# Kernel tuning notes

Measured on AMD Instinct MI355X. Metric: run time of the kernel, lower is better.

Reference implementation:

```python
import jax, jax.numpy as jnp
import numpy as np

N = 100000      # nodes
E = 1600000     # edges (avg degree 16)
IN = 512        # input feature dim
H, C = 8, 8     # conv1: 8 heads x 8 channels (hardcoded in module)
HID = H * C     # 64
OUT = 64        # output classes (conv2: 1 head, no concat)
NEG_SLOPE = 0.2 # PyG GATConv default leaky-relu slope


def setup_inputs() -> dict:
    key = jax.random.key(0)
    ks = jax.random.split(key, 10)
    x = jax.random.normal(ks[0], (N, IN), dtype=jnp.float32)
    edge_index = jax.random.randint(ks[1], (2, E), 0, N, dtype=jnp.int32)
    W1 = jax.random.normal(ks[2], (IN, HID), dtype=jnp.float32) / np.sqrt(IN).astype(np.float32)
    a_src1 = jax.random.normal(ks[3], (H, C), dtype=jnp.float32) * 0.1
    a_dst1 = jax.random.normal(ks[4], (H, C), dtype=jnp.float32) * 0.1
    b1 = jnp.zeros((HID,), dtype=jnp.float32)
    W2 = jax.random.normal(ks[5], (HID, OUT), dtype=jnp.float32) / np.sqrt(HID).astype(np.float32)
    a_src2 = jax.random.normal(ks[6], (1, OUT), dtype=jnp.float32) * 0.1
    a_dst2 = jax.random.normal(ks[7], (1, OUT), dtype=jnp.float32) * 0.1
    b2 = jnp.zeros((OUT,), dtype=jnp.float32)
    return {"x": x, "edge_index": edge_index, "W1": W1, "a_src1": a_src1,
            "a_dst1": a_dst1, "b1": b1, "W2": W2, "a_src2": a_src2,
            "a_dst2": a_dst2, "b2": b2}


def _gat_attend(h, src, dst, a_s, a_d, n_nodes):
    """h: [N,H,C]; src/dst: [E]; a_s/a_d: [H,C] -> aggregated [N,H,C]."""
    # per-node half-scores (PyG decomposition of a^T [Wx_i || Wx_j])
    sc_s = jnp.sum(h * a_s, axis=-1)                       # [N,H]
    sc_d = jnp.sum(h * a_d, axis=-1)                       # [N,H]
    logits = jax.nn.leaky_relu(sc_s[src] + sc_d[dst], NEG_SLOPE)  # [E,H]
    # segment softmax over edges grouped by destination node
    mx = jax.ops.segment_max(logits, dst, num_segments=n_nodes)   # [N,H]
    ex = jnp.exp(logits - mx[dst])                          # [E,H]
    denom = jax.ops.segment_sum(ex, dst, num_segments=n_nodes)    # [N,H]
    alpha = ex / (denom[dst] + 1e-16)                       # [E,H]
    msg = h[src] * alpha[:, :, None]                        # [E,H,C]
    return jax.ops.segment_sum(msg, dst, num_segments=n_nodes)    # [N,H,C]


def reference(x, edge_index, W1, a_src1, a_dst1, b1, W2, a_src2, a_dst2, b2):
    n = x.shape[0]
    loop = jnp.arange(n, dtype=edge_index.dtype)
    src = jnp.concatenate([edge_index[0], loop])            # self-loops (PyG default)
    dst = jnp.concatenate([edge_index[1], loop])
    # conv1: 8 heads, concat
    h1 = (x @ W1).reshape(n, H, C)
    o1 = _gat_attend(h1, src, dst, a_src1, a_dst1, n).reshape(n, HID) + b1
    x2 = jax.nn.elu(o1)
    # conv2: 1 head, no concat
    h2 = (x2 @ W2).reshape(n, 1, OUT)
    o2 = _gat_attend(h2, src, dst, a_src2, a_dst2, n)[:, 0] + b2
    return jax.nn.log_softmax(o2, axis=1)
```

## Files before the change

### kernel.cpp

```cpp
#include <hip/hip_runtime.h>
#include <cstdint>
#include <cstddef>

#define LEAKY 0.2f
#define NEG_INF -3.402823466e38f
static const int CHUNK = 2048;

typedef __attribute__((ext_vector_type(8))) short short8;
typedef __attribute__((ext_vector_type(4))) float floatx4;

__device__ __forceinline__ float dot4(float4 a, float4 b) {
    return a.x * b.x + a.y * b.y + a.z * b.z + a.w * b.w;
}

__device__ __forceinline__ unsigned short f2bf(float f) {
    unsigned u = __float_as_uint(f);
    u += 0x7fffu + ((u >> 16) & 1u);
    return (unsigned short)(u >> 16);
}
__device__ __forceinline__ float bf2f(unsigned short u) {
    return __uint_as_float(((unsigned)u) << 16);
}
__device__ __forceinline__ float bflo(unsigned u) { return __uint_as_float(u << 16); }
__device__ __forceinline__ float bfhi(unsigned u) { return __uint_as_float(u & 0xffff0000u); }

__global__ __launch_bounds__(256) void k_misc(const float* __restrict__ W1, unsigned short* __restrict__ W1t,
                                              int* __restrict__ deg, int Nn) {
    int i = blockIdx.x * 256 + threadIdx.x;
    if (i < 64 * 512) {
        int n = i >> 9, k = i & 511;
        W1t[i] = f2bf(W1[k * 64 + n]);
    }
    if (i < Nn) deg[i] = 1;
}

__global__ __launch_bounds__(256) void k_count_p(const int* __restrict__ ei, int* __restrict__ deg,
                                                 int E, int Nn) {
    int part = blockIdx.x & 7;
    int lo = (int)((long long)Nn * part >> 3);
    int hi = (int)((long long)Nn * (part + 1) >> 3);
    int nthr = (gridDim.x >> 3) * 256;
    int tid = (blockIdx.x >> 3) * 256 + threadIdx.x;
    for (int e = tid; e < E; e += nthr) {
        int d = ei[E + e];
        if (d >= lo && d < hi) atomicAdd(&deg[d], 1);
    }
}

__global__ __launch_bounds__(256) void k_scan1(const int* __restrict__ deg, int* __restrict__ bsum, int Nn) {
    __shared__ int sm[256];
    int b = blockIdx.x, t = threadIdx.x;
    int s = 0;
    int i0 = b * CHUNK + t * 8;
#pragma unroll
    for (int j = 0; j < 8; ++j) { int i = i0 + j; if (i < Nn) s += deg[i]; }
    sm[t] = s;
    __syncthreads();
    for (int o = 128; o; o >>= 1) { if (t < o) sm[t] += sm[t + o]; __syncthreads(); }
    if (t == 0) bsum[b] = sm[0];
}

__global__ __launch_bounds__(256) void k_scan3(const int* __restrict__ deg, const int* __restrict__ bsum,
                                               int* __restrict__ indptr, int* __restrict__ cursor,
                                               int Nn, int B) {
    __shared__ int wsum[4];
    int b = blockIdx.x, t = threadIdx.x, lane = t & 63, w = t >> 6;

    int vb = (lane < B) ? bsum[lane] : 0;
    int incb = vb;
#pragma unroll
    for (int o = 1; o < 64; o <<= 1) { int u = __shfl_up(incb, o); if (lane >= o) incb += u; }
    int bpre_b = __shfl(incb - vb, b);

    int i0 = b * CHUNK + t * 8;
    int d[8]; int s = 0;
#pragma unroll
    for (int j = 0; j < 8; ++j) { int i = i0 + j; d[j] = (i < Nn) ? deg[i] : 0; s += d[j]; }
    int inc = s;
#pragma unroll
    for (int o = 1; o < 64; o <<= 1) { int u = __shfl_up(inc, o); if (lane >= o) inc += u; }
    if (lane == 63) wsum[w] = inc;
    __syncthreads();
    int wofs = 0;
    for (int k = 0; k < w; ++k) wofs += wsum[k];
    int base = bpre_b + wofs + (inc - s);
    int run = 0;
#pragma unroll
    for (int j = 0; j < 8; ++j) {
        int i = i0 + j;
        if (i < Nn) {
            int v = base + run;
            indptr[i] = v; cursor[i] = v;
            run += d[j];
            if (i == Nn - 1) indptr[Nn] = v + d[j];
        }
    }
}

__global__ __launch_bounds__(256) void k_fill_p(const int* __restrict__ ei, int* __restrict__ cursor,
                                                int* __restrict__ csr, int E, int Nn) {
    int part = blockIdx.x & 7;
    int lo = (int)((long long)Nn * part >> 3);
    int hi = (int)((long long)Nn * (part + 1) >> 3);
    int nthr = (gridDim.x >> 3) * 256;
    int tid = (blockIdx.x >> 3) * 256 + threadIdx.x;
    int tot = E + Nn;
    for (int idx = tid; idx < tot; idx += nthr) {
        int d = (idx < E) ? ei[E + idx] : idx - E;
        if (d >= lo && d < hi) {
            int s = (idx < E) ? ei[idx] : idx - E;
            int slot = atomicAdd(&cursor[d], 1);
            csr[slot] = s;
        }
    }
}

__global__ __launch_bounds__(256) void gemm1_mfma(const float* __restrict__ A, const unsigned short* __restrict__ W1t,
                                                  unsigned short* __restrict__ C,
                                                  const float* __restrict__ as1, const float* __restrict__ ad1,
                                                  float* __restrict__ scs, float* __restrict__ scd, int M) {
    __shared__ __align__(16) unsigned short As[128][40];
    __shared__ __align__(16) unsigned short Bs[64][40];
    int t = threadIdx.x;
    int w = t >> 6, l = t & 63;
    int quad = l >> 4, lm = l & 15;
    int row0 = blockIdx.x * 128;

    floatx4 acc[2][4] = {};

    for (int k0 = 0; k0 < 512; k0 += 32) {
#pragma unroll
        for (int j = 0; j < 4; ++j) {
            int f = t + 256 * j;
            int r = f >> 3, c4 = f & 7;
            int rg = row0 + r; if (rg >= M) rg = M - 1;
            float4 v = *(const float4*)(A + (size_t)rg * 512 + k0 + c4 * 4);
            ushort4 b; b.x = f2bf(v.x); b.y = f2bf(v.y); b.z = f2bf(v.z); b.w = f2bf(v.w);
            *(ushort4*)&As[r][c4 * 4] = b;
        }
        {
            int n = t >> 2, seg = t & 3;
            *(uint4*)&Bs[n][seg * 8] = *(const uint4*)(W1t + (size_t)n * 512 + k0 + seg * 8);
        }
        __syncthreads();

        short8 af[2], bfm[4];
#pragma unroll
        for (int tm = 0; tm < 2; ++tm) {
            int m = w * 32 + tm * 16 + lm;
            af[tm] = *(const short8*)&As[m][quad * 8];
        }
#pragma unroll
        for (int tn = 0; tn < 4; ++tn) {
            int n = tn * 16 + lm;
            bfm[tn] = *(const short8*)&Bs[n][quad * 8];
        }
#pragma unroll
        for (int tm = 0; tm < 2; ++tm)
#pragma unroll
            for (int tn = 0; tn < 4; ++tn)
                acc[tm][tn] = __builtin_amdgcn_mfma_f32_16x16x32_bf16(af[tm], bfm[tn], acc[tm][tn], 0, 0, 0);
        __syncthreads();
    }

    float as_l[4], ad_l[4];
#pragma unroll
    for (int tn = 0; tn < 4; ++tn) { as_l[tn] = as1[tn * 16 + lm]; ad_l[tn] = ad1[tn * 16 + lm]; }
    int hbase = (l >> 3) & 1;

#pragma unroll
    for (int tm = 0; tm < 2; ++tm) {
#pragma unroll
        for (int r = 0; r < 4; ++r) {
            int row = row0 + w * 32 + tm * 16 + quad * 4 + r;
            if (row < M) {
#pragma unroll
                for (int tn = 0; tn < 4; ++tn)
                    C[(size_t)row * 64 + tn * 16 + lm] = f2bf(acc[tm][tn][r]);
                float ps[4], pd[4];
#pragma unroll
                for (int tn = 0; tn < 4; ++tn) {
                    ps[tn] = acc[tm][tn][r] * as_l[tn];
                    pd[tn] = acc[tm][tn][r] * ad_l[tn];
                }
#pragma unroll
                for (int o = 1; o < 8; o <<= 1) {
#pragma unroll
                    for (int tn = 0; tn < 4; ++tn) {
                        ps[tn] += __shfl_xor(ps[tn], o);
                        pd[tn] += __shfl_xor(pd[tn], o);
                    }
                }
                if ((l & 7) == 0) {
#pragma unroll
                    for (int tn = 0; tn < 4; ++tn) {
                        scs[(size_t)row * 8 + tn * 2 + hbase] = ps[tn];
                        scd[(size_t)row * 8 + tn * 2 + hbase] = pd[tn];
                    }
                }
            }
        }
    }
}

template <int KB>
__global__ __launch_bounds__(256) void gemm_n64(const float* __restrict__ A, const float* __restrict__ B,
                                                unsigned short* __restrict__ C,
                                                const float* __restrict__ as2, const float* __restrict__ ad2,
                                                float* __restrict__ sc2s, float* __restrict__ sc2d,
                                                int M, int K) {
    __shared__ float As[KB][68];
    __shared__ float Bs[KB][68];
    int tid = threadIdx.x;
    int row0 = blockIdx.x * 64;
    int tx = tid & 15, ty = tid >> 4;
    float acc[4][4] = {};
    for (int k0 = 0; k0 < K; k0 += KB) {
#pragma unroll
        for (int j = 0; j < (64 * KB) / (256 * 4); ++j) {
            int f = tid + 256 * j;
            int r = f / (KB / 4);
            int c4 = f % (KB / 4);
            int rg = row0 + r; if (rg >= M) rg = M - 1;
            float4 v = *(const float4*)(A + (size_t)rg * K + k0 + c4 * 4);
            As[c4 * 4 + 0][r] = v.x; As[c4 * 4 + 1][r] = v.y;
            As[c4 * 4 + 2][r] = v.z; As[c4 * 4 + 3][r] = v.w;
        }
#pragma unroll
        for (int j = 0; j < (KB * 64) / (256 * 4); ++j) {
            int f = tid + 256 * j;
            int kk = f / 16, c4 = f % 16;
            *(float4*)&Bs[kk][c4 * 4] = *(const float4*)(B + (size_t)(k0 + kk) * 64 + c4 * 4);
        }
        __syncthreads();
#pragma unroll
        for (int kk = 0; kk < KB; ++kk) {
            float4 a = *(const float4*)&As[kk][ty * 4];
            float4 b = *(const float4*)&Bs[kk][tx * 4];
            float av[4] = {a.x, a.y, a.z, a.w};
            float bv[4] = {b.x, b.y, b.z, b.w};
#pragma unroll
            for (int i = 0; i < 4; ++i)
#pragma unroll
                for (int j = 0; j < 4; ++j) acc[i][j] += av[i] * bv[j];
        }
        __syncthreads();
    }
    float as_l[4], ad_l[4];
#pragma unroll
    for (int j = 0; j < 4; ++j) { as_l[j] = as2[tx * 4 + j]; ad_l[j] = ad2[tx * 4 + j]; }
#pragma unroll
    for (int i = 0; i < 4; ++i) {
        int rg = row0 + ty * 4 + i;
        if (rg < M) {
            ushort4 b; b.x = f2bf(acc[i][0]); b.y = f2bf(acc[i][1]);
            b.z = f2bf(acc[i][2]); b.w = f2bf(acc[i][3]);
            *(ushort4*)(C + (size_t)rg * 64 + tx * 4) = b;
            float ps = acc[i][0] * as_l[0] + acc[i][1] * as_l[1] + acc[i][2] * as_l[2] + acc[i][3] * as_l[3];
            float pd = acc[i][0] * ad_l[0] + acc[i][1] * ad_l[1] + acc[i][2] * ad_l[2] + acc[i][3] * ad_l[3];
#pragma unroll
            for (int o = 1; o < 16; o <<= 1) { ps += __shfl_xor(ps, o); pd += __shfl_xor(pd, o); }
            if (tx == 0) { sc2s[rg] = ps; sc2d[rg] = pd; }
        }
    }
}

__global__ __launch_bounds__(256, 4) void k_agg1(const unsigned short* __restrict__ h1, const float* __restrict__ scs,
                                                 const float* __restrict__ scd, const int* __restrict__ indptr,
                                                 const int* __restrict__ csr, const float* __restrict__ b1,
                                                 float* __restrict__ x2, int Nn) {
    int node = (blockIdx.x * 256 + threadIdx.x) >> 6;
    int l = threadIdx.x & 63;
    if (node >= Nn) return;
    int h8 = l & 7, grp = l >> 3;
    int start = indptr[node], end = indptr[node + 1];
    float sd = scd[node * 8 + h8];

    float dsum = 0.f;
    float acc8[8] = {};
    for (int base = start; base < end; base += 64) {
        int e = base + l;
        int s64 = csr[e < end ? e : start];
        int cnt = min(64, end - base);
        int nb = (cnt + 7) >> 3;
        int sbv[8];
#pragma unroll
        for (int b = 0; b < 8; ++b) sbv[b] = __shfl(s64, b * 8 + grp);
        float exv[8];
#pragma unroll
        for (int b = 0; b < 8; ++b) {
            if (b < nb) {
                float v = scs[(size_t)sbv[b] * 8 + h8] + sd;
                v = v > 0.f ? v : LEAKY * v;
                exv[b] = (base + b * 8 + grp < end) ? __expf(v) : 0.f;
            }
        }
        uint4 q[8];
#pragma unroll
        for (int b = 0; b < 8; ++b)
            if (b < nb) q[b] = *(const uint4*)(h1 + (size_t)sbv[b] * 64 + h8 * 8);
#pragma unroll
        for (int b = 0; b < 8; ++b) {
            if (b < nb) {
                float ex = exv[b];
                dsum += ex;
                acc8[0] += ex * bflo(q[b].x); acc8[1] += ex * bfhi(q[b].x);
                acc8[2] += ex * bflo(q[b].y); acc8[3] += ex * bfhi(q[b].y);
                acc8[4] += ex * bflo(q[b].z); acc8[5] += ex * bfhi(q[b].z);
                acc8[6] += ex * bflo(q[b].w); acc8[7] += ex * bfhi(q[b].w);
            }
        }
    }
#pragma unroll
    for (int o = 8; o < 64; o <<= 1) {
        dsum += __shfl_xor(dsum, o);
#pragma unroll
        for (int k = 0; k < 8; ++k) acc8[k] += __shfl_xor(acc8[k], o);
    }
    if (grp == 0) {
        float inv = 1.f / (dsum + 1e-16f);
        float4 ba = *((const float4*)b1 + h8 * 2);
        float4 bb = *((const float4*)b1 + h8 * 2 + 1);
        float o0 = acc8[0] * inv + ba.x, o1 = acc8[1] * inv + ba.y;
        float o2 = acc8[2] * inv + ba.z, o3 = acc8[3] * inv + ba.w;
        float o4 = acc8[4] * inv + bb.x, o5 = acc8[5] * inv + bb.y;
        float o6 = acc8[6] * inv + bb.z, o7 = acc8[7] * inv + bb.w;
        o0 = o0 > 0.f ? o0 : expm1f(o0); o1 = o1 > 0.f ? o1 : expm1f(o1);
        o2 = o2 > 0.f ? o2 : expm1f(o2); o3 = o3 > 0.f ? o3 : expm1f(o3);
        o4 = o4 > 0.f ? o4 : expm1f(o4); o5 = o5 > 0.f ? o5 : expm1f(o5);
        o6 = o6 > 0.f ? o6 : expm1f(o6); o7 = o7 > 0.f ? o7 : expm1f(o7);
        float* dst = x2 + (size_t)node * 64 + h8 * 8;
        *(float4*)dst = make_float4(o0, o1, o2, o3);
        *(float4*)(dst + 4) = make_float4(o4, o5, o6, o7);
    }
}

__global__ __launch_bounds__(256, 4) void k_agg2(const unsigned short* __restrict__ h2, const float* __restrict__ scs,
                                                 const float* __restrict__ scd, const int* __restrict__ indptr,
                                                 const int* __restrict__ csr, const float* __restrict__ b2,
                                                 float* __restrict__ out, int Nn) {
    int node = (blockIdx.x * 256 + threadIdx.x) >> 6;
    int l = threadIdx.x & 63;
    if (node >= Nn) return;
    int g = l >> 3, c8 = l & 7;
    int start = indptr[node], end = indptr[node + 1];
    float sd = scd[node];

    float dsum = 0.f;
    float acc8[8] = {};
    for (int base = start; base < end; base += 64) {
        int e = base + l;
        int s64 = csr[e < end ? e : start];
        float v = scs[s64] + sd;
        v = v > 0.f ? v : LEAKY * v;
        float ex = (e < end) ? __expf(v) : 0.f;
        dsum += ex;
        int cnt = min(64, end - base);
        int nb = (cnt + 7) >> 3;
        float exv[8]; int sbv[8];
#pragma unroll
        for (int b = 0; b < 8; ++b) {
            exv[b] = __shfl(ex, b * 8 + g);
            sbv[b] = __shfl(s64, b * 8 + g);
        }
        uint4 q[8];
#pragma unroll
        for (int b = 0; b < 8; ++b)
            if (b < nb) q[b] = *(const uint4*)(h2 + (size_t)sbv[b] * 64 + c8 * 8);
#pragma unroll
        for (int b = 0; b < 8; ++b) {
            if (b < nb) {
                float exq = exv[b];
                acc8[0] += exq * bflo(q[b].x); acc8[1] += exq * bfhi(q[b].x);
                acc8[2] += exq * bflo(q[b].y); acc8[3] += exq * bfhi(q[b].y);
                acc8[4] += exq * bflo(q[b].z); acc8[5] += exq * bfhi(q[b].z);
                acc8[6] += exq * bflo(q[b].w); acc8[7] += exq * bfhi(q[b].w);
            }
        }
    }
#pragma unroll
    for (int o = 32; o; o >>= 1) dsum += __shfl_xor(dsum, o);
#pragma unroll
    for (int o = 8; o < 64; o <<= 1)
#pragma unroll
        for (int k = 0; k < 8; ++k) acc8[k] += __shfl_xor(acc8[k], o);

    float inv = 1.f / (dsum + 1e-16f);
    float4 ba = *((const float4*)b2 + c8 * 2);
    float4 bb = *((const float4*)b2 + c8 * 2 + 1);
    float ov[8];
    ov[0] = acc8[0] * inv + ba.x; ov[1] = acc8[1] * inv + ba.y;
    ov[2] = acc8[2] * inv + ba.z; ov[3] = acc8[3] * inv + ba.w;
    ov[4] = acc8[4] * inv + bb.x; ov[5] = acc8[5] * inv + bb.y;
    ov[6] = acc8[6] * inv + bb.z; ov[7] = acc8[7] * inv + bb.w;

    float m2 = ov[0];
#pragma unroll
    for (int k = 1; k < 8; ++k) m2 = fmaxf(m2, ov[k]);
#pragma unroll
    for (int o = 1; o < 8; o <<= 1) m2 = fmaxf(m2, __shfl_xor(m2, o));
    float se = 0.f;
#pragma unroll
    for (int k = 0; k < 8; ++k) se += __expf(ov[k] - m2);
#pragma unroll
    for (int o = 1; o < 8; o <<= 1) se += __shfl_xor(se, o);
    float ls = m2 + __logf(se);
    if (g == 0) {
        float* dst = out + (size_t)node * 64 + c8 * 8;
        *(float4*)dst = make_float4(ov[0] - ls, ov[1] - ls, ov[2] - ls, ov[3] - ls);
        *(float4*)(dst + 4) = make_float4(ov[4] - ls, ov[5] - ls, ov[6] - ls, ov[7] - ls);
    }
}

extern "C" void kernel_launch(void* const* d_in, const int* in_sizes, int n_in,
                              void* d_out, int out_size, void* d_ws, size_t ws_size,
                              hipStream_t stream) {
    (void)n_in; (void)out_size; (void)ws_size;
    const float* x   = (const float*)d_in[0];
    const int*   ei  = (const int*)d_in[1];
    const float* W1  = (const float*)d_in[2];
    const float* as1 = (const float*)d_in[3];
    const float* ad1 = (const float*)d_in[4];
    const float* b1  = (const float*)d_in[5];
    const float* W2  = (const float*)d_in[6];
    const float* as2 = (const float*)d_in[7];
    const float* ad2 = (const float*)d_in[8];
    const float* b2  = (const float*)d_in[9];
    float* out = (float*)d_out;

    const int N = in_sizes[0] / 512;
    const int E = in_sizes[1] / 2;

    char* p = (char*)d_ws;
    auto alloc = [&](size_t bytes) -> char* {
        char* r = p; p += (bytes + 255) & ~(size_t)255; return r;
    };
    unsigned short* h1bf = (unsigned short*)alloc((size_t)N * 64 * 2);
    float* x2    = (float*)alloc((size_t)N * 64 * 4);
    unsigned short* h2bf = h1bf;
    float* sc1s  = (float*)alloc((size_t)N * 8 * 4);
    float* sc1d  = (float*)alloc((size_t)N * 8 * 4);
    float* sc2s  = (float*)alloc((size_t)N * 4);
    float* sc2d  = (float*)alloc((size_t)N * 4);
    int*   deg   = (int*)alloc((size_t)N * 4);
    int*   cursor= (int*)alloc((size_t)N * 4);
    int*   indptr= (int*)alloc((size_t)(N + 1) * 4);
    int*   csr   = (int*)alloc((size_t)(E + N) * 4);
    int*   bsum  = (int*)alloc(64 * 4);
    unsigned short* W1t = (unsigned short*)alloc(64 * 512 * 2);

    const int B = (N + CHUNK - 1) / CHUNK;

    const int miscGrid = (((64 * 512) > N ? (64 * 512) : N) + 255) / 256;
    k_misc<<<miscGrid, 256, 0, stream>>>(W1, W1t, deg, N);

    k_count_p<<<1024, 256, 0, stream>>>(ei, deg, E, N);
    k_scan1  <<<B, 256, 0, stream>>>(deg, bsum, N);
    k_scan3  <<<B, 256, 0, stream>>>(deg, bsum, indptr, cursor, N, B);
    k_fill_p <<<1024, 256, 0, stream>>>(ei, cursor, csr, E, N);

    gemm1_mfma<<<(N + 127) / 128, 256, 0, stream>>>(x, W1t, h1bf, as1, ad1, sc1s, sc1d, N);
    k_agg1<<<(N + 3) / 4, 256, 0, stream>>>(h1bf, sc1s, sc1d, indptr, csr, b1, x2, N);

    gemm_n64<64><<<(N + 63) / 64, 256, 0, stream>>>(x2, W2, h2bf, as2, ad2, sc2s, sc2d, N, 64);
    k_agg2<<<(N + 3) / 4, 256, 0, stream>>>(h2bf, sc2s, sc2d, indptr, csr, b2, out, N);
}
```

Measured before the change: 649.8 us.

## Merge degree counting into GEMM1 launch and simplify aggregation loops

The degree-count pass now runs as extra blocks in the same launch as the layer-1 MFMA GEMM, so the memory-bound edge scan overlaps the compute-bound GEMM and one kernel launch goes away. Separately, both aggregation kernels drop the staged batch of 8 gather loads in favour of simpler per-batch loops, and their occupancy hint in the launch bounds is removed. The loop change lowers register pressure but gives up memory-level parallelism in the gathers, so the two edits pull in different directions on the latency-bound aggregation.

```diff
diff --git a/kernel.cpp b/kernel.cpp
--- a/kernel.cpp
+++ b/kernel.cpp
@@ -8,10 +8,6 @@
 
 typedef __attribute__((ext_vector_type(8))) short short8;
 typedef __attribute__((ext_vector_type(4))) float floatx4;
-
-__device__ __forceinline__ float dot4(float4 a, float4 b) {
-    return a.x * b.x + a.y * b.y + a.z * b.z + a.w * b.w;
-}
 
 __device__ __forceinline__ unsigned short f2bf(float f) {
     unsigned u = __float_as_uint(f);
@@ -34,16 +30,108 @@
     if (i < Nn) deg[i] = 1;
 }
 
-__global__ __launch_bounds__(256) void k_count_p(const int* __restrict__ ei, int* __restrict__ deg,
-                                                 int E, int Nn) {
-    int part = blockIdx.x & 7;
-    int lo = (int)((long long)Nn * part >> 3);
-    int hi = (int)((long long)Nn * (part + 1) >> 3);
-    int nthr = (gridDim.x >> 3) * 256;
-    int tid = (blockIdx.x >> 3) * 256 + threadIdx.x;
-    for (int e = tid; e < E; e += nthr) {
-        int d = ei[E + e];
-        if (d >= lo && d < hi) atomicAdd(&deg[d], 1);
+__global__ __launch_bounds__(256) void k_mega1(const float* __restrict__ A, const unsigned short* __restrict__ W1t,
+                                               unsigned short* __restrict__ C,
+                                               const float* __restrict__ as1, const float* __restrict__ ad1,
+                                               float* __restrict__ scs, float* __restrict__ scd, int M,
+                                               const int* __restrict__ ei, int* __restrict__ deg, int E, int G1) {
+    __shared__ __align__(16) unsigned short As[128][40];
+    __shared__ __align__(16) unsigned short Bs[64][40];
+
+    if ((int)blockIdx.x >= G1) {
+        int cb = blockIdx.x - G1;
+        int part = cb & 7;
+        int Nn = M;
+        int lo = (int)((long long)Nn * part >> 3);
+        int hi = (int)((long long)Nn * (part + 1) >> 3);
+        int nthr = (1024 >> 3) * 256;
+        int tid = (cb >> 3) * 256 + threadIdx.x;
+        for (int e = tid; e < E; e += nthr) {
+            int d = ei[E + e];
+            if (d >= lo && d < hi) atomicAdd(&deg[d], 1);
+        }
+        return;
+    }
+
+    int t = threadIdx.x;
+    int w = t >> 6, l = t & 63;
+    int quad = l >> 4, lm = l & 15;
+    int row0 = blockIdx.x * 128;
+
+    floatx4 acc[2][4] = {};
+
+    for (int k0 = 0; k0 < 512; k0 += 32) {
+#pragma unroll
+        for (int j = 0; j < 4; ++j) {
+            int f = t + 256 * j;
+            int r = f >> 3, c4 = f & 7;
+            int rg = row0 + r; if (rg >= M) rg = M - 1;
+            float4 v = *(const float4*)(A + (size_t)rg * 512 + k0 + c4 * 4);
+            ushort4 b; b.x = f2bf(v.x); b.y = f2bf(v.y); b.z = f2bf(v.z); b.w = f2bf(v.w);
+            *(ushort4*)&As[r][c4 * 4] = b;
+        }
+        {
+            int n = t >> 2, seg = t & 3;
+            *(uint4*)&Bs[n][seg * 8] = *(const uint4*)(W1t + (size_t)n * 512 + k0 + seg * 8);
+        }
+        __syncthreads();
+
+        short8 af[2], bfm[4];
+#pragma unroll
+        for (int tm = 0; tm < 2; ++tm) {
+            int m = w * 32 + tm * 16 + lm;
+            af[tm] = *(const short8*)&As[m][quad * 8];
+        }
+#pragma unroll
+        for (int tn = 0; tn < 4; ++tn) {
+            int n = tn * 16 + lm;
+            bfm[tn] = *(const short8*)&Bs[n][quad * 8];
+        }
+#pragma unroll
+        for (int tm = 0; tm < 2; ++tm)
+#pragma unroll
+            for (int tn = 0; tn < 4; ++tn)
+                acc[tm][tn] = __builtin_amdgcn_mfma_f32_16x16x32_bf16(af[tm], bfm[tn], acc[tm][tn], 0, 0, 0);
+        __syncthreads();
+    }
+
+    float as_l[4], ad_l[4];
+#pragma unroll
+    for (int tn = 0; tn < 4; ++tn) { as_l[tn] = as1[tn * 16 + lm]; ad_l[tn] = ad1[tn * 16 + lm]; }
+    int hbase = (l >> 3) & 1;
+
+#pragma unroll
+    for (int tm = 0; tm < 2; ++tm) {
+#pragma unroll
+        for (int r = 0; r < 4; ++r) {
+            int row = row0 + w * 32 + tm * 16 + quad * 4 + r;
+            if (row < M) {
+#pragma unroll
+                for (int tn = 0; tn < 4; ++tn)
+                    C[(size_t)row * 64 + tn * 16 + lm] = f2bf(acc[tm][tn][r]);
+                float ps[4], pd[4];
+#pragma unroll
+                for (int tn = 0; tn < 4; ++tn) {
+                    ps[tn] = acc[tm][tn][r] * as_l[tn];
+                    pd[tn] = acc[tm][tn][r] * ad_l[tn];
+                }
+#pragma unroll
+                for (int o = 1; o < 8; o <<= 1) {
+#pragma unroll
+                    for (int tn = 0; tn < 4; ++tn) {
+                        ps[tn] += __shfl_xor(ps[tn], o);
+                        pd[tn] += __shfl_xor(pd[tn], o);
+                    }
+                }
+                if ((l & 7) == 0) {
+#pragma unroll
+                    for (int tn = 0; tn < 4; ++tn) {
+                        scs[(size_t)row * 8 + tn * 2 + hbase] = ps[tn];
+                        scd[(size_t)row * 8 + tn * 2 + hbase] = pd[tn];
+                    }
+                }
+            }
+        }
     }
 }
 
@@ -115,94 +203,6 @@
     }
 }
 
-__global__ __launch_bounds__(256) void gemm1_mfma(const float* __restrict__ A, const unsigned short* __restrict__ W1t,
-                                                  unsigned short* __restrict__ C,
-                                                  const float* __restrict__ as1, const float* __restrict__ ad1,
-                                                  float* __restrict__ scs, float* __restrict__ scd, int M) {
-    __shared__ __align__(16) unsigned short As[128][40];
-    __shared__ __align__(16) unsigned short Bs[64][40];
-    int t = threadIdx.x;
-    int w = t >> 6, l = t & 63;
-    int quad = l >> 4, lm = l & 15;
-    int row0 = blockIdx.x * 128;
-
-    floatx4 acc[2][4] = {};
-
-    for (int k0 = 0; k0 < 512; k0 += 32) {
-#pragma unroll
-        for (int j = 0; j < 4; ++j) {
-            int f = t + 256 * j;
-            int r = f >> 3, c4 = f & 7;
-            int rg = row0 + r; if (rg >= M) rg = M - 1;
-            float4 v = *(const float4*)(A + (size_t)rg * 512 + k0 + c4 * 4);
-            ushort4 b; b.x = f2bf(v.x); b.y = f2bf(v.y); b.z = f2bf(v.z); b.w = f2bf(v.w);
-            *(ushort4*)&As[r][c4 * 4] = b;
-        }
-        {
-            int n = t >> 2, seg = t & 3;
-            *(uint4*)&Bs[n][seg * 8] = *(const uint4*)(W1t + (size_t)n * 512 + k0 + seg * 8);
-        }
-        __syncthreads();
-
-        short8 af[2], bfm[4];
-#pragma unroll
-        for (int tm = 0; tm < 2; ++tm) {
-            int m = w * 32 + tm * 16 + lm;
-            af[tm] = *(const short8*)&As[m][quad * 8];
-        }
-#pragma unroll
-        for (int tn = 0; tn < 4; ++tn) {
-            int n = tn * 16 + lm;
-            bfm[tn] = *(const short8*)&Bs[n][quad * 8];
-        }
-#pragma unroll
-        for (int tm = 0; tm < 2; ++tm)
-#pragma unroll
-            for (int tn = 0; tn < 4; ++tn)
-                acc[tm][tn] = __builtin_amdgcn_mfma_f32_16x16x32_bf16(af[tm], bfm[tn], acc[tm][tn], 0, 0, 0);
-        __syncthreads();
-    }
-
-    float as_l[4], ad_l[4];
-#pragma unroll
-    for (int tn = 0; tn < 4; ++tn) { as_l[tn] = as1[tn * 16 + lm]; ad_l[tn] = ad1[tn * 16 + lm]; }
-    int hbase = (l >> 3) & 1;
-
-#pragma unroll
-    for (int tm = 0; tm < 2; ++tm) {
-#pragma unroll
-        for (int r = 0; r < 4; ++r) {
-            int row = row0 + w * 32 + tm * 16 + quad * 4 + r;
-            if (row < M) {
-#pragma unroll
-                for (int tn = 0; tn < 4; ++tn)
-                    C[(size_t)row * 64 + tn * 16 + lm] = f2bf(acc[tm][tn][r]);
-                float ps[4], pd[4];
-#pragma unroll
-                for (int tn = 0; tn < 4; ++tn) {
-                    ps[tn] = acc[tm][tn][r] * as_l[tn];
-                    pd[tn] = acc[tm][tn][r] * ad_l[tn];
-                }
-#pragma unroll
-                for (int o = 1; o < 8; o <<= 1) {
-#pragma unroll
-                    for (int tn = 0; tn < 4; ++tn) {
-                        ps[tn] += __shfl_xor(ps[tn], o);
-                        pd[tn] += __shfl_xor(pd[tn], o);
-                    }
-                }
-                if ((l & 7) == 0) {
-#pragma unroll
-                    for (int tn = 0; tn < 4; ++tn) {
-                        scs[(size_t)row * 8 + tn * 2 + hbase] = ps[tn];
-                        scd[(size_t)row * 8 + tn * 2 + hbase] = pd[tn];
-                    }
-                }
-            }
-        }
-    }
-}
-
 template <int KB>
 __global__ __launch_bounds__(256) void gemm_n64(const float* __restrict__ A, const float* __restrict__ B,
                                                 unsigned short* __restrict__ C,
@@ -265,10 +265,10 @@
     }
 }
 
-__global__ __launch_bounds__(256, 4) void k_agg1(const unsigned short* __restrict__ h1, const float* __restrict__ scs,
-                                                 const float* __restrict__ scd, const int* __restrict__ indptr,
-                                                 const int* __restrict__ csr, const float* __restrict__ b1,
-                                                 float* __restrict__ x2, int Nn) {
+__global__ __launch_bounds__(256) void k_agg1(const unsigned short* __restrict__ h1, const float* __restrict__ scs,
+                                              const float* __restrict__ scd, const int* __restrict__ indptr,
+                                              const int* __restrict__ csr, const float* __restrict__ b1,
+                                              float* __restrict__ x2, int Nn) {
     int node = (blockIdx.x * 256 + threadIdx.x) >> 6;
     int l = threadIdx.x & 63;
     if (node >= Nn) return;
@@ -283,31 +283,20 @@
         int s64 = csr[e < end ? e : start];
         int cnt = min(64, end - base);
         int nb = (cnt + 7) >> 3;
-        int sbv[8];
-#pragma unroll
-        for (int b = 0; b < 8; ++b) sbv[b] = __shfl(s64, b * 8 + grp);
-        float exv[8];
 #pragma unroll
         for (int b = 0; b < 8; ++b) {
             if (b < nb) {
-                float v = scs[(size_t)sbv[b] * 8 + h8] + sd;
+                int slot = base + b * 8 + grp;
+                int sb = __shfl(s64, b * 8 + grp);
+                float v = scs[sb * 8 + h8] + sd;
                 v = v > 0.f ? v : LEAKY * v;
-                exv[b] = (base + b * 8 + grp < end) ? __expf(v) : 0.f;
-            }
-        }
-        uint4 q[8];
-#pragma unroll
-        for (int b = 0; b < 8; ++b)
-            if (b < nb) q[b] = *(const uint4*)(h1 + (size_t)sbv[b] * 64 + h8 * 8);
-#pragma unroll
-        for (int b = 0; b < 8; ++b) {
-            if (b < nb) {
-                float ex = exv[b];
+                float ex = (slot < end) ? __expf(v) : 0.f;
                 dsum += ex;
-                acc8[0] += ex * bflo(q[b].x); acc8[1] += ex * bfhi(q[b].x);
-                acc8[2] += ex * bflo(q[b].y); acc8[3] += ex * bfhi(q[b].y);
-                acc8[4] += ex * bflo(q[b].z); acc8[5] += ex * bfhi(q[b].z);
-                acc8[6] += ex * bflo(q[b].w); acc8[7] += ex * bfhi(q[b].w);
+                uint4 q = *(const uint4*)(h1 + (size_t)sb * 64 + h8 * 8);
+                acc8[0] += ex * bflo(q.x); acc8[1] += ex * bfhi(q.x);
+                acc8[2] += ex * bflo(q.y); acc8[3] += ex * bfhi(q.y);
+                acc8[4] += ex * bflo(q.z); acc8[5] += ex * bfhi(q.z);
+                acc8[6] += ex * bflo(q.w); acc8[7] += ex * bfhi(q.w);
             }
         }
     }
@@ -335,10 +324,10 @@
     }
 }
 
-__global__ __launch_bounds__(256, 4) void k_agg2(const unsigned short* __restrict__ h2, const float* __restrict__ scs,
-                                                 const float* __restrict__ scd, const int* __restrict__ indptr,
-                                                 const int* __restrict__ csr, const float* __restrict__ b2,
-                                                 float* __restrict__ out, int Nn) {
+__global__ __launch_bounds__(256) void k_agg2(const unsigned short* __restrict__ h2, const float* __restrict__ scs,
+                                              const float* __restrict__ scd, const int* __restrict__ indptr,
+                                              const int* __restrict__ csr, const float* __restrict__ b2,
+                                              float* __restrict__ out, int Nn) {
     int node = (blockIdx.x * 256 + threadIdx.x) >> 6;
     int l = threadIdx.x & 63;
     if (node >= Nn) return;
@@ -357,25 +346,15 @@
         dsum += ex;
         int cnt = min(64, end - base);
         int nb = (cnt + 7) >> 3;
-        float exv[8]; int sbv[8];
-#pragma unroll
-        for (int b = 0; b < 8; ++b) {
-            exv[b] = __shfl(ex, b * 8 + g);
-            sbv[b] = __shfl(s64, b * 8 + g);
-        }
-        uint4 q[8];
-#pragma unroll
-        for (int b = 0; b < 8; ++b)
-            if (b < nb) q[b] = *(const uint4*)(h2 + (size_t)sbv[b] * 64 + c8 * 8);
-#pragma unroll
-        for (int b = 0; b < 8; ++b) {
-            if (b < nb) {
-                float exq = exv[b];
-                acc8[0] += exq * bflo(q[b].x); acc8[1] += exq * bfhi(q[b].x);
-                acc8[2] += exq * bflo(q[b].y); acc8[3] += exq * bfhi(q[b].y);
-                acc8[4] += exq * bflo(q[b].z); acc8[5] += exq * bfhi(q[b].z);
-                acc8[6] += exq * bflo(q[b].w); acc8[7] += exq * bfhi(q[b].w);
-            }
+#pragma unroll 2
+        for (int b = 0; b < nb; ++b) {
+            float exv = __shfl(ex, b * 8 + g);
+            int sb = __shfl(s64, b * 8 + g);
+            uint4 q = *(const uint4*)(h2 + (size_t)sb * 64 + c8 * 8);
+            acc8[0] += exv * bflo(q.x); acc8[1] += exv * bfhi(q.x);
+            acc8[2] += exv * bflo(q.y); acc8[3] += exv * bfhi(q.y);
+            acc8[4] += exv * bflo(q.z); acc8[5] += exv * bfhi(q.z);
+            acc8[6] += exv * bflo(q.w); acc8[7] += exv * bfhi(q.w);
         }
     }
 #pragma unroll
@@ -450,18 +429,21 @@
     unsigned short* W1t = (unsigned short*)alloc(64 * 512 * 2);
 
     const int B = (N + CHUNK - 1) / CHUNK;
+    const int G1 = (N + 127) / 128;
 
     const int miscGrid = (((64 * 512) > N ? (64 * 512) : N) + 255) / 256;
     k_misc<<<miscGrid, 256, 0, stream>>>(W1, W1t, deg, N);
 
-    k_count_p<<<1024, 256, 0, stream>>>(ei, deg, E, N);
-    k_scan1  <<<B, 256, 0, stream>>>(deg, bsum, N);
-    k_scan3  <<<B, 256, 0, stream>>>(deg, bsum, indptr, cursor, N, B);
-    k_fill_p <<<1024, 256, 0, stream>>>(ei, cursor, csr, E, N);
-
-    gemm1_mfma<<<(N + 127) / 128, 256, 0, stream>>>(x, W1t, h1bf, as1, ad1, sc1s, sc1d, N);
+    k_mega1<<<G1 + 1024, 256, 0, stream>>>(x, W1t, h1bf, as1, ad1, sc1s, sc1d, N,
+                                           ei, deg, E, G1);
+
+    k_scan1 <<<B, 256, 0, stream>>>(deg, bsum, N);
+    k_scan3 <<<B, 256, 0, stream>>>(deg, bsum, indptr, cursor, N, B);
+    k_fill_p<<<1024, 256, 0, stream>>>(ei, cursor, csr, E, N);
+
     k_agg1<<<(N + 3) / 4, 256, 0, stream>>>(h1bf, sc1s, sc1d, indptr, csr, b1, x2, N);
 
     gemm_n64<64><<<(N + 63) / 64, 256, 0, stream>>>(x2, W2, h2bf, as2, ad2, sc2s, sc2d, N, 64);
+
     k_agg2<<<(N + 3) / 4, 256, 0, stream>>>(h2bf, sc2s, sc2d, indptr, csr, b2, out, N);
 }
```

Result: faster. 592.1 us (-8.9%).
